# Optimization experiments

Hardware: AMD Instinct MI355X
Metric: run time of the kernel (lower is better)

The kernel has to match this reference:

```python
import jax, jax.numpy as jnp
import numpy as np


def setup_inputs() -> dict:
    key = jax.random.key(0)
    ks = jax.random.split(key, 4)
    N, T, D, H = 64, 512, 1024, 1024
    x = jax.random.normal(ks[0], (N, T, D), dtype=jnp.float32)
    h0 = jax.random.normal(ks[1], (N, H), dtype=jnp.float32)
    Wx = jax.random.normal(ks[2], (D, 4 * H), dtype=jnp.float32) / np.sqrt(D)
    Wh = jax.random.normal(ks[3], (H, 4 * H), dtype=jnp.float32) / np.sqrt(H)
    b = jnp.zeros((4 * H,), dtype=jnp.float32)
    return {"x": x, "h0": h0, "Wx": Wx, "Wh": Wh, "b": b}


def reference(x, h0, Wx, Wh, b):
    # x: [N, T, D]; h0: [N, H]; Wx: [D, 4H]; Wh: [H, 4H]; b: [4H]
    H = h0.shape[1]
    # Batch the input-to-hidden matmul over all timesteps at once: [N, T, 4H]
    xW = jnp.einsum('ntd,df->ntf', x, Wx) + b
    c0 = jnp.zeros_like(h0)

    def step(carry, xw_t):
        prev_h, prev_c = carry
        preact = xw_t + prev_h @ Wh           # [N, 4H]
        ai, af, ao, ag = jnp.split(preact, 4, axis=1)
        i = jax.nn.sigmoid(ai)
        f = jax.nn.sigmoid(af)
        o = jax.nn.sigmoid(ao)
        g = jnp.tanh(ag)
        next_c = f * prev_c + i * g
        next_h = o * jnp.tanh(next_c)
        return (next_h, next_c), next_h

    # scan over time: move T to leading axis
    _, hs = jax.lax.scan(step, (h0, c0), jnp.swapaxes(xW, 0, 1))
    return jnp.swapaxes(hs, 0, 1)  # [N, T, H]
```

## Files before the change

### kernel.cpp

```cpp
#include <hip/hip_runtime.h>
#include <cstdint>
#include <cstddef>

#define N_ 64
#define T_ 512
#define D_ 1024
#define H_ 1024
#define FH 4096

typedef __attribute__((ext_vector_type(8))) short bf16x8;
typedef __attribute__((ext_vector_type(4))) float f32x4;

static __device__ __forceinline__ uint16_t f2bf_(float f) {
  union { float f; uint32_t u; } v; v.f = f;
  uint32_t u = v.u + 0x7FFFu + ((v.u >> 16) & 1u);
  return (uint16_t)(u >> 16);
}
static __device__ __forceinline__ float bf2f_(uint16_t s) {
  union { uint32_t u; float f; } v; v.u = ((uint32_t)s) << 16;
  return v.f;
}
static __device__ __forceinline__ void unpk2_(unsigned long long e,
                                              uint32_t& hi, uint32_t& lo) {
  uint32_t a = (uint32_t)e, b = (uint32_t)(e >> 32);
  hi = (a >> 16) | (b & 0xFFFF0000u);
  lo = (a & 0xFFFFu) | (b << 16);
}

#define ALD(p) (*(p))

__global__ __launch_bounds__(256) void pack_w_k(const float* __restrict__ W,
                                                ushort* __restrict__ hi,
                                                ushort* __restrict__ lo) {
  const int i = blockIdx.x * 256 + threadIdx.x;
  const int lane = i & 63, kc = (i >> 6) & 31, bid = i >> 11;
  const int c = lane & 15;
  const int col = (c >> 2) * H_ + (bid << 2) + (c & 3);
  const int k0 = (kc << 5) + ((lane >> 4) << 3);
  const size_t o = ((size_t)(bid * 32 + kc) * 64 + lane) * 8;
#pragma unroll
  for (int e = 0; e < 8; ++e) {
    float v = W[(size_t)(k0 + e) * FH + col];
    ushort h = f2bf_(v);
    hi[o + e] = h;
    lo[o + e] = f2bf_(v - bf2f_(h));
  }
}

__global__ __launch_bounds__(256) void split_f32_k(const float* __restrict__ src,
                                                   ushort* __restrict__ hi,
                                                   ushort* __restrict__ lo) {
  const size_t i = (size_t)blockIdx.x * 256 + threadIdx.x;
  float4 v = reinterpret_cast<const float4*>(src)[i];
  ushort4 h, l;
  h.x = f2bf_(v.x); l.x = f2bf_(v.x - bf2f_(h.x));
  h.y = f2bf_(v.y); l.y = f2bf_(v.y - bf2f_(h.y));
  h.z = f2bf_(v.z); l.z = f2bf_(v.z - bf2f_(h.z));
  h.w = f2bf_(v.w); l.w = f2bf_(v.w - bf2f_(h.w));
  reinterpret_cast<ushort4*>(hi)[i] = h;
  reinterpret_cast<ushort4*>(lo)[i] = l;
}

__global__ __launch_bounds__(256) void conv_h0pk_k(const float* __restrict__ src,
                                                   uint32_t* __restrict__ dst,
                                                   unsigned* bar) {
  if (blockIdx.x == 0) {
    bar[threadIdx.x] = 0u;
    if (threadIdx.x < 8) bar[384 + 32 * threadIdx.x] = 0u;
  }
  const int i = blockIdx.x * 256 + threadIdx.x;
  float4 v = reinterpret_cast<const float4*>(src)[i];
  uint4 o;
  { ushort h = f2bf_(v.x); o.x = ((uint32_t)h << 16) | f2bf_(v.x - bf2f_(h)); }
  { ushort h = f2bf_(v.y); o.y = ((uint32_t)h << 16) | f2bf_(v.y - bf2f_(h)); }
  { ushort h = f2bf_(v.z); o.z = ((uint32_t)h << 16) | f2bf_(v.z - bf2f_(h)); }
  { ushort h = f2bf_(v.w); o.w = ((uint32_t)h << 16) | f2bf_(v.w - bf2f_(h)); }
  reinterpret_cast<uint4*>(dst)[i] = o;
}

__global__ __launch_bounds__(256, 3) void gemm_xw_mfma(
    const ushort* __restrict__ Wxh, const ushort* __restrict__ Wxl,
    const ushort* __restrict__ xh, const ushort* __restrict__ xl,
    const float* __restrict__ bias, uint32_t* __restrict__ xwp, int tb) {
  const int bid = blockIdx.y;
  const int tl = blockIdx.x << 2;
  const int t0 = tb + tl;
  const int tid = threadIdx.x, lane = tid & 63, mt = tid >> 6;
  const int row = (mt << 4) | (lane & 15);
  const int kg = lane >> 4;

  const bf16x8* Bh = reinterpret_cast<const bf16x8*>(Wxh) + (size_t)bid * 2048 + lane;
  const bf16x8* Bl = reinterpret_cast<const bf16x8*>(Wxl) + (size_t)bid * 2048 + lane;
  const ushort* ah = xh + ((size_t)row * T_ + t0) * D_ + (kg << 3);
  const ushort* al = xl + ((size_t)row * T_ + t0) * D_ + (kg << 3);

  f32x4 aA0 = {0.f, 0.f, 0.f, 0.f}, aB0 = {0.f, 0.f, 0.f, 0.f}, aC0 = {0.f, 0.f, 0.f, 0.f};
  f32x4 aA1 = {0.f, 0.f, 0.f, 0.f}, aB1 = {0.f, 0.f, 0.f, 0.f}, aC1 = {0.f, 0.f, 0.f, 0.f};
  f32x4 aA2 = {0.f, 0.f, 0.f, 0.f}, aB2 = {0.f, 0.f, 0.f, 0.f}, aC2 = {0.f, 0.f, 0.f, 0.f};
  f32x4 aA3 = {0.f, 0.f, 0.f, 0.f}, aB3 = {0.f, 0.f, 0.f, 0.f}, aC3 = {0.f, 0.f, 0.f, 0.f};
#pragma unroll 2
  for (int kc = 0; kc < 32; ++kc) {
    bf16x8 bh = Bh[kc << 6];
    bf16x8 bl = Bl[kc << 6];
    bf16x8 h0 = *reinterpret_cast<const bf16x8*>(ah + (kc << 5));
    bf16x8 l0 = *reinterpret_cast<const bf16x8*>(al + (kc << 5));
    bf16x8 h1 = *reinterpret_cast<const bf16x8*>(ah + D_ + (kc << 5));
    bf16x8 l1 = *reinterpret_cast<const bf16x8*>(al + D_ + (kc << 5));
    bf16x8 h2 = *reinterpret_cast<const bf16x8*>(ah + 2 * D_ + (kc << 5));
    bf16x8 l2 = *reinterpret_cast<const bf16x8*>(al + 2 * D_ + (kc << 5));
    bf16x8 h3 = *reinterpret_cast<const bf16x8*>(ah + 3 * D_ + (kc << 5));
    bf16x8 l3 = *reinterpret_cast<const bf16x8*>(al + 3 * D_ + (kc << 5));
    aA0 = __builtin_amdgcn_mfma_f32_16x16x32_bf16(h0, bh, aA0, 0, 0, 0);
    aA1 = __builtin_amdgcn_mfma_f32_16x16x32_bf16(h1, bh, aA1, 0, 0, 0);
    aA2 = __builtin_amdgcn_mfma_f32_16x16x32_bf16(h2, bh, aA2, 0, 0, 0);
    aA3 = __builtin_amdgcn_mfma_f32_16x16x32_bf16(h3, bh, aA3, 0, 0, 0);
    aB0 = __builtin_amdgcn_mfma_f32_16x16x32_bf16(h0, bl, aB0, 0, 0, 0);
    aB1 = __builtin_amdgcn_mfma_f32_16x16x32_bf16(h1, bl, aB1, 0, 0, 0);
    aB2 = __builtin_amdgcn_mfma_f32_16x16x32_bf16(h2, bl, aB2, 0, 0, 0);
    aB3 = __builtin_amdgcn_mfma_f32_16x16x32_bf16(h3, bl, aB3, 0, 0, 0);
    aC0 = __builtin_amdgcn_mfma_f32_16x16x32_bf16(l0, bh, aC0, 0, 0, 0);
    aC1 = __builtin_amdgcn_mfma_f32_16x16x32_bf16(l1, bh, aC1, 0, 0, 0);
    aC2 = __builtin_amdgcn_mfma_f32_16x16x32_bf16(l2, bh, aC2, 0, 0, 0);
    aC3 = __builtin_amdgcn_mfma_f32_16x16x32_bf16(l3, bh, aC3, 0, 0, 0);
  }
  f32x4 xa0 = (aA0 + aB0) + aC0;
  f32x4 xa1 = (aA1 + aB1) + aC1;
  f32x4 xa2 = (aA2 + aB2) + aC2;
  f32x4 xa3 = (aA3 + aB3) + aC3;

  const int dc = lane & 15, dr = (lane >> 4) << 2;
  const int g = dc >> 2, jj = dc & 3;
  const float bv = bias[g * H_ + (bid << 2) + jj];
#pragma unroll
  for (int r = 0; r < 4; ++r) {
    const int rw = (mt << 4) + dr + r;
    const size_t o = ((size_t)tl * 256 + bid) * 1024 + rw * 16 + jj * 4 + g;
    float v0 = xa0[r] + bv, v1 = xa1[r] + bv, v2 = xa2[r] + bv, v3 = xa3[r] + bv;
    ushort h;
    h = f2bf_(v0); xwp[o] = ((uint32_t)h << 16) | f2bf_(v0 - bf2f_(h));
    h = f2bf_(v1); xwp[o + 262144] = ((uint32_t)h << 16) | f2bf_(v1 - bf2f_(h));
    h = f2bf_(v2); xwp[o + 2 * 262144] = ((uint32_t)h << 16) | f2bf_(v2 - bf2f_(h));
    h = f2bf_(v3); xwp[o + 3 * 262144] = ((uint32_t)h << 16) | f2bf_(v3 - bf2f_(h));
  }
}

__global__ __launch_bounds__(512, 2) void lstm_scan_k(
    const ushort* __restrict__ Whh_g, const ushort* __restrict__ Whl_g,
    const uint32_t* __restrict__ xwp,
    uint32_t* __restrict__ hseq, float* __restrict__ cbuf,
    float* __restrict__ out, unsigned* __restrict__ bar, int tb) {
  extern __shared__ char ldsraw[];
  bf16x8* const WhH = (bf16x8*)ldsraw;
  bf16x8* const WhL = WhH + 2048;
  float* const pre = (float*)(WhL + 2048);

  const int tid = threadIdx.x, bid = blockIdx.x;
  const int lane = tid & 63, w = tid >> 6;
  const int mt = w & 3, kh = w >> 2;
  const int khb = kh << 4;
  const int arow = (mt << 4) | (lane & 15);
  const int kg = lane >> 4;
  const int dc = lane & 15, dr = (lane >> 4) << 2;
  const int en = tid >> 2, ejj = tid & 3;

  unsigned* const relmy = bar + 384 + ((bid & 7) << 5);

  {
    const bf16x8* gh = reinterpret_cast<const bf16x8*>(Whh_g) + (size_t)bid * 2048;
    const bf16x8* gl = reinterpret_cast<const bf16x8*>(Whl_g) + (size_t)bid * 2048;
#pragma unroll
    for (int r = 0; r < 4; ++r) {
      int u = tid + (r << 9);
      WhH[u] = gh[u];
      WhL[u] = gl[u];
    }
  }
  __syncthreads();

  for (int tl = 0; tl < 128; ++tl) {
    const int t = tb + tl;
    f32x4 acc0 = {0.f, 0.f, 0.f, 0.f};
    f32x4 acc1 = {0.f, 0.f, 0.f, 0.f};
    const unsigned long long* Apk =
        (const unsigned long long*)(hseq + (size_t)t * 65536) +
        arow * 512 + (kh << 8) + kg * 4;

    unsigned long long pa0, pa1, pa2, pa3, pb0, pb1, pb2, pb3;
    unsigned long long pc0, pc1, pc2, pc3, pd0, pd1, pd2, pd3;
    unsigned long long qa0, qa1, qa2, qa3, qb0, qb1, qb2, qb3;
    unsigned long long qc0, qc1, qc2, qc3, qd0, qd1, qd2, qd3;

#define HLD(P, CH)                                                            \
  {                                                                           \
    const unsigned long long* ap_ = Apk + ((CH) << 6);                        \
    P##a0 = ALD(ap_ + 0);  P##a1 = ALD(ap_ + 1);                              \
    P##a2 = ALD(ap_ + 2);  P##a3 = ALD(ap_ + 3);                              \
    P##b0 = ALD(ap_ + 16); P##b1 = ALD(ap_ + 17);                             \
    P##b2 = ALD(ap_ + 18); P##b3 = ALD(ap_ + 19);                             \
    P##c0 = ALD(ap_ + 32); P##c1 = ALD(ap_ + 33);                             \
    P##c2 = ALD(ap_ + 34); P##c3 = ALD(ap_ + 35);                             \
    P##d0 = ALD(ap_ + 48); P##d1 = ALD(ap_ + 49);                             \
    P##d2 = ALD(ap_ + 50); P##d3 = ALD(ap_ + 51);                             \
  }

#define HKC(E0, E1, E2, E3, KCG, ACC)                                         \
  {                                                                           \
    union { uint32_t u[4]; bf16x8 v; } fh_, fl_;                              \
    unpk2_(E0, fh_.u[0], fl_.u[0]);                                           \
    unpk2_(E1, fh_.u[1], fl_.u[1]);                                           \
    unpk2_(E2, fh_.u[2], fl_.u[2]);                                           \
    unpk2_(E3, fh_.u[3], fl_.u[3]);                                           \
    bf16x8 bh_ = WhH[((KCG) << 6) + lane];                                    \
    bf16x8 bl_ = WhL[((KCG) << 6) + lane];                                    \
    ACC = __builtin_amdgcn_mfma_f32_16x16x32_bf16(fh_.v, bh_, ACC, 0, 0, 0);  \
    ACC = __builtin_amdgcn_mfma_f32_16x16x32_bf16(fh_.v, bl_, ACC, 0, 0, 0);  \
    ACC = __builtin_amdgcn_mfma_f32_16x16x32_bf16(fl_.v, bh_, ACC, 0, 0, 0);  \
  }

#define HCOMP(P, CH)                                                          \
  HKC(P##a0, P##a1, P##a2, P##a3, khb + (CH) * 4 + 0, acc0)                   \
  HKC(P##b0, P##b1, P##b2, P##b3, khb + (CH) * 4 + 1, acc1)                   \
  HKC(P##c0, P##c1, P##c2, P##c3, khb + (CH) * 4 + 2, acc0)                   \
  HKC(P##d0, P##d1, P##d2, P##d3, khb + (CH) * 4 + 3, acc1)

    HLD(p, 0)
    HLD(q, 1) HCOMP(p, 0)
    HLD(p, 2) HCOMP(q, 1)
    HLD(q, 3) HCOMP(p, 2)
    HCOMP(q, 3)
#undef HLD
#undef HKC
#undef HCOMP

    f32x4 accs = acc0 + acc1;
#pragma unroll
    for (int r = 0; r < 4; ++r)
      pre[((kh << 6) + (mt << 4) + dr + r) * 17 + dc] = accs[r];
    __syncthreads();

    if (tid < 256) {
      const uint4 xp = *reinterpret_cast<const uint4*>(
          xwp + (size_t)tl * 262144 + (size_t)bid * 1024 + en * 16 + ejj * 4);
      float a0 = pre[en * 17 + ejj] + pre[(64 + en) * 17 + ejj] +
                 bf2f_((ushort)(xp.x >> 16)) + bf2f_((ushort)(xp.x & 0xFFFF));
      float a1 = pre[en * 17 + 4 + ejj] + pre[(64 + en) * 17 + 4 + ejj] +
                 bf2f_((ushort)(xp.y >> 16)) + bf2f_((ushort)(xp.y & 0xFFFF));
      float a2 = pre[en * 17 + 8 + ejj] + pre[(64 + en) * 17 + 8 + ejj] +
                 bf2f_((ushort)(xp.z >> 16)) + bf2f_((ushort)(xp.z & 0xFFFF));
      float a3 = pre[en * 17 + 12 + ejj] + pre[(64 + en) * 17 + 12 + ejj] +
                 bf2f_((ushort)(xp.w >> 16)) + bf2f_((ushort)(xp.w & 0xFFFF));
      const int hx = en * H_ + (bid << 2) + ejj;
      float cp = (t == 0) ? 0.f : cbuf[hx];
      float iv = 1.f / (1.f + __expf(-a0));
      float fv = 1.f / (1.f + __expf(-a1));
      float ov = 1.f / (1.f + __expf(-a2));
      float gv = tanhf(a3);
      float cn = fmaf(fv, cp, iv * gv);
      cbuf[hx] = cn;
      float hn = ov * tanhf(cn);
      out[(size_t)en * ((size_t)T_ * H_) + (size_t)t * H_ + (bid << 2) + ejj] = hn;
      ushort hh = f2bf_(hn);
      uint32_t pk = ((uint32_t)hh << 16) | f2bf_(hn - bf2f_(hh));
      __hip_atomic_store(&hseq[(size_t)(t + 1) * 65536 + hx], pk,
                         __ATOMIC_RELAXED, __HIP_MEMORY_SCOPE_AGENT);
    }

    asm volatile("s_waitcnt vmcnt(0)" ::: "memory");
    __syncthreads();

    const unsigned tgt = (unsigned)(t + 1);
    if (tid == 0)
      __hip_atomic_store(&bar[bid], tgt, __ATOMIC_RELAXED,
                         __HIP_MEMORY_SCOPE_AGENT);
    if (bid == 0 && tid < 64) {
      const unsigned long long* fl = (const unsigned long long*)bar;
      for (;;) {
        unsigned long long v0 = __hip_atomic_load(fl + tid, __ATOMIC_RELAXED,
                                                  __HIP_MEMORY_SCOPE_AGENT);
        unsigned long long v1 = __hip_atomic_load(fl + 64 + tid, __ATOMIC_RELAXED,
                                                  __HIP_MEMORY_SCOPE_AGENT);
        bool ok = ((unsigned)v0 >= tgt) && ((unsigned)(v0 >> 32) >= tgt) &&
                  ((unsigned)v1 >= tgt) && ((unsigned)(v1 >> 32) >= tgt);
        if (__all((int)ok)) break;
      }
      if (tid < 8)
        __hip_atomic_store(bar + 384 + (tid << 5), tgt, __ATOMIC_RELAXED,
                           __HIP_MEMORY_SCOPE_AGENT);
    }
    if (tid == 0) {
      while (__hip_atomic_load(relmy, __ATOMIC_RELAXED,
                               __HIP_MEMORY_SCOPE_AGENT) < tgt)
        __builtin_amdgcn_s_sleep(1);
    }
    __syncthreads();
  }
}

__global__ __launch_bounds__(256) void lstm_step_fb(
    const float* __restrict__ xt, const float* __restrict__ Wx,
    const float* __restrict__ Wh, const float* __restrict__ bias,
    const float* __restrict__ h_prev, long long hstride,
    float* __restrict__ cbuf, float* __restrict__ h_out, int first) {
  __shared__ float hS[32][128];
  __shared__ float wT[32][132];
  __shared__ float pre[32][34];
  const int tid = threadIdx.x;
  const int colblk = blockIdx.x & 127;
  const int nh = blockIdx.x >> 7;
  const int j0 = colblk << 3;
  const int n0 = nh << 5;
  const int ng = tid >> 4, cg2 = tid & 15;
  const int na = ng << 1, ca = cg2 << 1;

  float acc[2][2] = {{0.f, 0.f}, {0.f, 0.f}};

#pragma unroll
  for (int pr = 0; pr < 2; ++pr) {
    const float* src = (pr == 0) ? h_prev : xt;
    long long sstr = (pr == 0) ? hstride : (long long)T_ * D_;
    const float* W = (pr == 0) ? Wh : Wx;
    for (int k0 = 0; k0 < 1024; k0 += 128) {
      __syncthreads();
#pragma unroll
      for (int p = 0; p < 4; ++p) {
        int idx = tid + (p << 8);
        int r = idx >> 5, c4 = (idx & 31) << 2;
        *reinterpret_cast<float4*>(&hS[r][c4]) =
            *reinterpret_cast<const float4*>(src + (size_t)(n0 + r) * sstr + k0 + c4);
      }
#pragma unroll
      for (int p = 0; p < 4; ++p) {
        int idx = tid + (p << 8);
        int k = idx >> 3, sub = idx & 7;
        int g = sub >> 1, hf = (sub & 1) << 2;
        float4 v = *reinterpret_cast<const float4*>(
            W + (size_t)(k0 + k) * FH + g * H_ + j0 + hf);
        int cb = (g << 3) + hf;
        wT[cb][k] = v.x; wT[cb + 1][k] = v.y; wT[cb + 2][k] = v.z; wT[cb + 3][k] = v.w;
      }
      __syncthreads();
#pragma unroll
      for (int kk = 0; kk < 128; kk += 4) {
        float4 h0v = *reinterpret_cast<const float4*>(&hS[na][kk]);
        float4 h1v = *reinterpret_cast<const float4*>(&hS[na + 1][kk]);
        float4 w0 = *reinterpret_cast<const float4*>(&wT[ca][kk]);
        float4 w1 = *reinterpret_cast<const float4*>(&wT[ca + 1][kk]);
        acc[0][0] = fmaf(h0v.x, w0.x, acc[0][0]); acc[0][0] = fmaf(h0v.y, w0.y, acc[0][0]);
        acc[0][0] = fmaf(h0v.z, w0.z, acc[0][0]); acc[0][0] = fmaf(h0v.w, w0.w, acc[0][0]);
        acc[0][1] = fmaf(h0v.x, w1.x, acc[0][1]); acc[0][1] = fmaf(h0v.y, w1.y, acc[0][1]);
        acc[0][1] = fmaf(h0v.z, w1.z, acc[0][1]); acc[0][1] = fmaf(h0v.w, w1.w, acc[0][1]);
        acc[1][0] = fmaf(h1v.x, w0.x, acc[1][0]); acc[1][0] = fmaf(h1v.y, w0.y, acc[1][0]);
        acc[1][0] = fmaf(h1v.z, w0.z, acc[1][0]); acc[1][0] = fmaf(h1v.w, w0.w, acc[1][0]);
        acc[1][1] = fmaf(h1v.x, w1.x, acc[1][1]); acc[1][1] = fmaf(h1v.y, w1.y, acc[1][1]);
        acc[1][1] = fmaf(h1v.z, w1.z, acc[1][1]); acc[1][1] = fmaf(h1v.w, w1.w, acc[1][1]);
      }
    }
  }

  pre[na][ca] = acc[0][0];
  pre[na][ca + 1] = acc[0][1];
  pre[na + 1][ca] = acc[1][0];
  pre[na + 1][ca + 1] = acc[1][1];
  __syncthreads();

  const int nl = tid >> 3, jl = tid & 7;
  const int n = n0 + nl;
  const int jg = j0 + jl;
  float ai = pre[nl][jl] + bias[jg];
  float af = pre[nl][8 + jl] + bias[H_ + jg];
  float ao = pre[nl][16 + jl] + bias[2 * H_ + jg];
  float ag = pre[nl][24 + jl] + bias[3 * H_ + jg];
  float cp = first ? 0.0f : cbuf[n * H_ + jg];
  float iv = 1.f / (1.f + __expf(-ai));
  float fv = 1.f / (1.f + __expf(-af));
  float ov = 1.f / (1.f + __expf(-ao));
  float gv = tanhf(ag);
  float cn = fmaf(fv, cp, iv * gv);
  cbuf[n * H_ + jg] = cn;
  h_out[(size_t)n * ((size_t)T_ * H_) + jg] = ov * tanhf(cn);
}

extern "C" void kernel_launch(void* const* d_in, const int* in_sizes, int n_in,
                              void* d_out, int out_size, void* d_ws, size_t ws_size,
                              hipStream_t stream) {
  (void)in_sizes; (void)n_in; (void)out_size;
  const float* x  = (const float*)d_in[0];
  const float* h0 = (const float*)d_in[1];
  const float* Wx = (const float*)d_in[2];
  const float* Wh = (const float*)d_in[3];
  const float* b  = (const float*)d_in[4];
  float* out = (float*)d_out;

  const size_t MB = 1u << 20;
  char* p = (char*)d_ws;

  if (ws_size >= 420 * MB) {
    unsigned* bar = (unsigned*)p;
    ushort* Whh = (ushort*)(p + 1 * MB);
    ushort* Whl = (ushort*)(p + 9 * MB);
    ushort* Wxh = (ushort*)(p + 17 * MB);
    ushort* Wxl = (ushort*)(p + 25 * MB);
    uint32_t* hseq = (uint32_t*)(p + 33 * MB);
    float* cbuf = (float*)(p + 162 * MB);
    ushort* xh = (ushort*)(p + 163 * MB);
    ushort* xl = (ushort*)(p + 227 * MB);
    uint32_t* xwp = (uint32_t*)(p + 291 * MB);

    pack_w_k<<<dim3(2048), dim3(256), 0, stream>>>(Wh, Whh, Whl);
    pack_w_k<<<dim3(2048), dim3(256), 0, stream>>>(Wx, Wxh, Wxl);
    split_f32_k<<<dim3(32768), dim3(256), 0, stream>>>(x, xh, xl);
    conv_h0pk_k<<<dim3(64), dim3(256), 0, stream>>>(h0, hseq, bar);

    const unsigned SH = 2048 * 16 * 2 + 128 * 17 * 4;
    hipFuncSetAttribute((const void*)lstm_scan_k,
                        hipFuncAttributeMaxDynamicSharedMemorySize, (int)SH);

    for (int c = 0; c < 4; ++c) {
      const int tb = c * 128;
      gemm_xw_mfma<<<dim3(32, 256), dim3(256), 0, stream>>>(Wxh, Wxl, xh, xl,
                                                            b, xwp, tb);
      lstm_scan_k<<<dim3(256), dim3(512), SH, stream>>>(Whh, Whl, xwp, hseq,
                                                        cbuf, out, bar, tb);
    }
  } else {
    float* cbuf = (float*)p;
    for (int t = 0; t < T_; ++t) {
      const float* hp = (t == 0) ? h0 : out + (size_t)(t - 1) * H_;
      long long hstr = (t == 0) ? (long long)H_ : (long long)T_ * H_;
      lstm_step_fb<<<dim3(256), dim3(256), 0, stream>>>(
          x + (size_t)t * D_, Wx, Wh, b, hp, hstr, cbuf,
          out + (size_t)t * H_, t == 0);
    }
  }
}
```

Measured before the change: 9.093 ms.

## Overlap next chunk's input GEMM with the LSTM scan in a fused kernel

The scan kernel gains 256 extra blocks that compute the input projection for the next time chunk while the first 256 blocks run the recurrence on the current chunk. xW is double-buffered between two workspace buffers, and the chunk length drops from 128 to 64 steps. This hides the standalone GEMM launches behind the latency-bound recurrence. The risks are that the GEMM blocks compete for CU resources and memory bandwidth with the barrier-synchronised scan blocks, and that the tighter launch bounds (512 threads, 4 blocks) may cause register spills.

```diff
diff --git a/kernel.cpp b/kernel.cpp
--- a/kernel.cpp
+++ b/kernel.cpp
@@ -7,6 +7,7 @@
 #define D_ 1024
 #define H_ 1024
 #define FH 4096
+#define CH 64
 
 typedef __attribute__((ext_vector_type(8))) short bf16x8;
 typedef __attribute__((ext_vector_type(4))) float f32x4;
@@ -78,26 +79,22 @@
   reinterpret_cast<uint4*>(dst)[i] = o;
 }
 
-__global__ __launch_bounds__(256, 3) void gemm_xw_mfma(
+static __device__ __forceinline__ void gemm4_(
     const ushort* __restrict__ Wxh, const ushort* __restrict__ Wxl,
     const ushort* __restrict__ xh, const ushort* __restrict__ xl,
-    const float* __restrict__ bias, uint32_t* __restrict__ xwp, int tb) {
-  const int bid = blockIdx.y;
-  const int tl = blockIdx.x << 2;
-  const int t0 = tb + tl;
-  const int tid = threadIdx.x, lane = tid & 63, mt = tid >> 6;
+    const float* __restrict__ bias, uint32_t* __restrict__ xwp,
+    int gbid, int tl, int t0, int lane, int mt) {
   const int row = (mt << 4) | (lane & 15);
   const int kg = lane >> 4;
-
-  const bf16x8* Bh = reinterpret_cast<const bf16x8*>(Wxh) + (size_t)bid * 2048 + lane;
-  const bf16x8* Bl = reinterpret_cast<const bf16x8*>(Wxl) + (size_t)bid * 2048 + lane;
+  const bf16x8* Bh = reinterpret_cast<const bf16x8*>(Wxh) + (size_t)gbid * 2048 + lane;
+  const bf16x8* Bl = reinterpret_cast<const bf16x8*>(Wxl) + (size_t)gbid * 2048 + lane;
   const ushort* ah = xh + ((size_t)row * T_ + t0) * D_ + (kg << 3);
   const ushort* al = xl + ((size_t)row * T_ + t0) * D_ + (kg << 3);
 
-  f32x4 aA0 = {0.f, 0.f, 0.f, 0.f}, aB0 = {0.f, 0.f, 0.f, 0.f}, aC0 = {0.f, 0.f, 0.f, 0.f};
-  f32x4 aA1 = {0.f, 0.f, 0.f, 0.f}, aB1 = {0.f, 0.f, 0.f, 0.f}, aC1 = {0.f, 0.f, 0.f, 0.f};
-  f32x4 aA2 = {0.f, 0.f, 0.f, 0.f}, aB2 = {0.f, 0.f, 0.f, 0.f}, aC2 = {0.f, 0.f, 0.f, 0.f};
-  f32x4 aA3 = {0.f, 0.f, 0.f, 0.f}, aB3 = {0.f, 0.f, 0.f, 0.f}, aC3 = {0.f, 0.f, 0.f, 0.f};
+  f32x4 aA0 = {0.f,0.f,0.f,0.f}, aB0 = {0.f,0.f,0.f,0.f}, aC0 = {0.f,0.f,0.f,0.f};
+  f32x4 aA1 = {0.f,0.f,0.f,0.f}, aB1 = {0.f,0.f,0.f,0.f}, aC1 = {0.f,0.f,0.f,0.f};
+  f32x4 aA2 = {0.f,0.f,0.f,0.f}, aB2 = {0.f,0.f,0.f,0.f}, aC2 = {0.f,0.f,0.f,0.f};
+  f32x4 aA3 = {0.f,0.f,0.f,0.f}, aB3 = {0.f,0.f,0.f,0.f}, aC3 = {0.f,0.f,0.f,0.f};
 #pragma unroll 2
   for (int kc = 0; kc < 32; ++kc) {
     bf16x8 bh = Bh[kc << 6];
@@ -130,11 +127,11 @@
 
   const int dc = lane & 15, dr = (lane >> 4) << 2;
   const int g = dc >> 2, jj = dc & 3;
-  const float bv = bias[g * H_ + (bid << 2) + jj];
+  const float bv = bias[g * H_ + (gbid << 2) + jj];
 #pragma unroll
   for (int r = 0; r < 4; ++r) {
     const int rw = (mt << 4) + dr + r;
-    const size_t o = ((size_t)tl * 256 + bid) * 1024 + rw * 16 + jj * 4 + g;
+    const size_t o = ((size_t)tl * 256 + gbid) * 1024 + rw * 16 + jj * 4 + g;
     float v0 = xa0[r] + bv, v1 = xa1[r] + bv, v2 = xa2[r] + bv, v3 = xa3[r] + bv;
     ushort h;
     h = f2bf_(v0); xwp[o] = ((uint32_t)h << 16) | f2bf_(v0 - bf2f_(h));
@@ -144,18 +141,45 @@
   }
 }
 
-__global__ __launch_bounds__(512, 2) void lstm_scan_k(
+__global__ __launch_bounds__(256, 3) void gemm_xw_mfma(
+    const ushort* __restrict__ Wxh, const ushort* __restrict__ Wxl,
+    const ushort* __restrict__ xh, const ushort* __restrict__ xl,
+    const float* __restrict__ bias, uint32_t* __restrict__ xwp, int tb) {
+  const int tl = blockIdx.x << 2;
+  gemm4_(Wxh, Wxl, xh, xl, bias, xwp, blockIdx.y, tl, tb + tl,
+         threadIdx.x & 63, threadIdx.x >> 6);
+}
+
+__global__ __launch_bounds__(512, 4) void lstm_fused_k(
     const ushort* __restrict__ Whh_g, const ushort* __restrict__ Whl_g,
-    const uint32_t* __restrict__ xwp,
+    const ushort* __restrict__ Wxh, const ushort* __restrict__ Wxl,
+    const ushort* __restrict__ xh, const ushort* __restrict__ xl,
+    const float* __restrict__ bias,
+    const uint32_t* __restrict__ xw_cur, uint32_t* __restrict__ xw_nxt,
     uint32_t* __restrict__ hseq, float* __restrict__ cbuf,
     float* __restrict__ out, unsigned* __restrict__ bar, int tb) {
   extern __shared__ char ldsraw[];
+  const int tid = threadIdx.x;
+  const int lane = tid & 63, w = tid >> 6;
+
+  if (blockIdx.x >= 256) {
+    const int tbn = tb + CH;
+    if (tbn >= T_) return;
+    const int gbid = blockIdx.x - 256;
+    const int mt = w & 3, sub = w >> 2;
+#pragma unroll 1
+    for (int tg = 0; tg < 8; ++tg) {
+      const int tl = (tg << 3) + (sub << 2);
+      gemm4_(Wxh, Wxl, xh, xl, bias, xw_nxt, gbid, tl, tbn + tl, lane, mt);
+    }
+    return;
+  }
+
   bf16x8* const WhH = (bf16x8*)ldsraw;
   bf16x8* const WhL = WhH + 2048;
   float* const pre = (float*)(WhL + 2048);
 
-  const int tid = threadIdx.x, bid = blockIdx.x;
-  const int lane = tid & 63, w = tid >> 6;
+  const int bid = blockIdx.x;
   const int mt = w & 3, kh = w >> 2;
   const int khb = kh << 4;
   const int arow = (mt << 4) | (lane & 15);
@@ -177,7 +201,7 @@
   }
   __syncthreads();
 
-  for (int tl = 0; tl < 128; ++tl) {
+  for (int tl = 0; tl < CH; ++tl) {
     const int t = tb + tl;
     f32x4 acc0 = {0.f, 0.f, 0.f, 0.f};
     f32x4 acc1 = {0.f, 0.f, 0.f, 0.f};
@@ -190,9 +214,9 @@
     unsigned long long qa0, qa1, qa2, qa3, qb0, qb1, qb2, qb3;
     unsigned long long qc0, qc1, qc2, qc3, qd0, qd1, qd2, qd3;
 
-#define HLD(P, CH)                                                            \
+#define HLD(P, CHk)                                                           \
   {                                                                           \
-    const unsigned long long* ap_ = Apk + ((CH) << 6);                        \
+    const unsigned long long* ap_ = Apk + ((CHk) << 6);                       \
     P##a0 = ALD(ap_ + 0);  P##a1 = ALD(ap_ + 1);                              \
     P##a2 = ALD(ap_ + 2);  P##a3 = ALD(ap_ + 3);                              \
     P##b0 = ALD(ap_ + 16); P##b1 = ALD(ap_ + 17);                             \
@@ -217,11 +241,11 @@
     ACC = __builtin_amdgcn_mfma_f32_16x16x32_bf16(fl_.v, bh_, ACC, 0, 0, 0);  \
   }
 
-#define HCOMP(P, CH)                                                          \
-  HKC(P##a0, P##a1, P##a2, P##a3, khb + (CH) * 4 + 0, acc0)                   \
-  HKC(P##b0, P##b1, P##b2, P##b3, khb + (CH) * 4 + 1, acc1)                   \
-  HKC(P##c0, P##c1, P##c2, P##c3, khb + (CH) * 4 + 2, acc0)                   \
-  HKC(P##d0, P##d1, P##d2, P##d3, khb + (CH) * 4 + 3, acc1)
+#define HCOMP(P, CHk)                                                         \
+  HKC(P##a0, P##a1, P##a2, P##a3, khb + (CHk) * 4 + 0, acc0)                  \
+  HKC(P##b0, P##b1, P##b2, P##b3, khb + (CHk) * 4 + 1, acc1)                  \
+  HKC(P##c0, P##c1, P##c2, P##c3, khb + (CHk) * 4 + 2, acc0)                  \
+  HKC(P##d0, P##d1, P##d2, P##d3, khb + (CHk) * 4 + 3, acc1)
 
     HLD(p, 0)
     HLD(q, 1) HCOMP(p, 0)
@@ -240,7 +264,7 @@
 
     if (tid < 256) {
       const uint4 xp = *reinterpret_cast<const uint4*>(
-          xwp + (size_t)tl * 262144 + (size_t)bid * 1024 + en * 16 + ejj * 4);
+          xw_cur + (size_t)tl * 262144 + (size_t)bid * 1024 + en * 16 + ejj * 4);
       float a0 = pre[en * 17 + ejj] + pre[(64 + en) * 17 + ejj] +
                  bf2f_((ushort)(xp.x >> 16)) + bf2f_((ushort)(xp.x & 0xFFFF));
       float a1 = pre[en * 17 + 4 + ejj] + pre[(64 + en) * 17 + 4 + ejj] +
@@ -404,7 +428,8 @@
     float* cbuf = (float*)(p + 162 * MB);
     ushort* xh = (ushort*)(p + 163 * MB);
     ushort* xl = (ushort*)(p + 227 * MB);
-    uint32_t* xwp = (uint32_t*)(p + 291 * MB);
+    uint32_t* xwp0 = (uint32_t*)(p + 291 * MB);
+    uint32_t* xwp1 = (uint32_t*)(p + 355 * MB);
 
     pack_w_k<<<dim3(2048), dim3(256), 0, stream>>>(Wh, Whh, Whl);
     pack_w_k<<<dim3(2048), dim3(256), 0, stream>>>(Wx, Wxh, Wxl);
@@ -412,15 +437,17 @@
     conv_h0pk_k<<<dim3(64), dim3(256), 0, stream>>>(h0, hseq, bar);
 
     const unsigned SH = 2048 * 16 * 2 + 128 * 17 * 4;
-    hipFuncSetAttribute((const void*)lstm_scan_k,
+    hipFuncSetAttribute((const void*)lstm_fused_k,
                         hipFuncAttributeMaxDynamicSharedMemorySize, (int)SH);
 
-    for (int c = 0; c < 4; ++c) {
-      const int tb = c * 128;
-      gemm_xw_mfma<<<dim3(32, 256), dim3(256), 0, stream>>>(Wxh, Wxl, xh, xl,
-                                                            b, xwp, tb);
-      lstm_scan_k<<<dim3(256), dim3(512), SH, stream>>>(Whh, Whl, xwp, hseq,
-                                                        cbuf, out, bar, tb);
+    gemm_xw_mfma<<<dim3(16, 256), dim3(256), 0, stream>>>(Wxh, Wxl, xh, xl, b,
+                                                          xwp0, 0);
+    for (int c = 0; c < 8; ++c) {
+      uint32_t* cur = (c & 1) ? xwp1 : xwp0;
+      uint32_t* nxt = (c & 1) ? xwp0 : xwp1;
+      lstm_fused_k<<<dim3(512), dim3(512), SH, stream>>>(
+          Whh, Whl, Wxh, Wxl, xh, xl, b, cur, nxt, hseq, cbuf, out, bar,
+          c * CH);
     }
   } else {
     float* cbuf = (float*)p;
```

Measured after the change: 8.027 ms (median of 2 runs). -11.7%, faster.
